# Performance work log

Hardware: AMD Instinct MI355X
Metric: run time of the kernel (lower is better)

The kernel has to match this reference:

```python
import jax, jax.numpy as jnp
import numpy as np

H = 4096        # hidden_size
NH = 32         # heads
HD = H // NH    # head_dim = 128
EPS = 1e-5
MINUS_INF = -10000.0
B, S = 2, 1024


def setup_inputs() -> dict:
    key = jax.random.key(0)
    ks = jax.random.split(key, 7)
    x = jax.random.normal(ks[0], (B, S, H), jnp.float32)
    mask = jnp.zeros((B, 1, 1, S), jnp.float32)  # additive padding mask (0 = keep)
    norm_w = 1.0 + 0.02 * jax.random.normal(ks[1], (H,), jnp.float32)
    norm_b = 0.02 * jax.random.normal(ks[2], (H,), jnp.float32)
    qkv_w = 0.02 * jax.random.normal(ks[3], (H, 3 * H), jnp.float32)
    qkv_b = 0.02 * jax.random.normal(ks[4], (3 * H,), jnp.float32)
    attn_ow = 0.02 * jax.random.normal(ks[5], (H, H), jnp.float32)
    return {"x": x, "mask": mask, "norm_w": norm_w, "norm_b": norm_b,
            "qkv_w": qkv_w, "qkv_b": qkv_b, "attn_ow": attn_ow}


def reference(x, mask, norm_w, norm_b, qkv_w, qkv_b, attn_ow):
    b, s, h = x.shape
    # --- pre-attention layernorm (qkv_gemm fuses this in DeepSpeed) ---
    mu = jnp.mean(x, axis=-1, keepdims=True)
    var = jnp.mean(jnp.square(x - mu), axis=-1, keepdims=True)
    inp_norm = (x - mu) * jax.lax.rsqrt(var + EPS) * norm_w + norm_b
    # --- fused QKV GEMM + bias ---
    qkv = inp_norm @ qkv_w + qkv_b                      # [b, s, 3H]
    q, k, v = jnp.split(qkv, 3, axis=-1)
    q = q.reshape(b, s, NH, HD).transpose(0, 2, 1, 3)   # [b, nh, s, hd]
    k = k.reshape(b, s, NH, HD).transpose(0, 2, 1, 3)
    v = v.reshape(b, s, NH, HD).transpose(0, 2, 1, 3)
    # --- scaled dot-product with triangular (causal) mask + additive input mask ---
    norm_factor = 1.0 / jnp.sqrt(jnp.asarray(HD, x.dtype))
    scores = jnp.einsum('bhqd,bhkd->bhqk', q, k) * norm_factor  # [b, nh, s, s]
    causal = jnp.where(jnp.tril(jnp.ones((s, s), bool)), 0.0, MINUS_INF).astype(x.dtype)
    probs = jax.nn.softmax(scores + causal + mask, axis=-1)
    ctx = jnp.einsum('bhqk,bhkd->bhqd', probs, v)               # [b, nh, s, hd]
    ctx = ctx.transpose(0, 2, 1, 3).reshape(b, s, h)
    # --- output projection (vector_matmul, bias applied later in MLP residual-add) ---
    out = ctx @ attn_ow
    return out
```

## Files before the change

### kernel.cpp

```cpp
#include <hip/hip_runtime.h>
#include <stdint.h>


#define S_LEN 1024
#define HID   4096
#define NHEAD 32
#define HDIM  128

typedef __attribute__((ext_vector_type(8))) short bf16x8;
typedef __attribute__((ext_vector_type(4))) float f32x4;
typedef __attribute__((ext_vector_type(8))) unsigned short us8;

__device__ __forceinline__ unsigned short f2bf(float f) {
    union { float f; unsigned u; } v; v.f = f;
    unsigned r = v.u + 0x7fffu + ((v.u >> 16) & 1u);
    return (unsigned short)(r >> 16);
}

__device__ __forceinline__ void gld16(const unsigned short* g, unsigned short* l) {
    __builtin_amdgcn_global_load_lds(
        (const __attribute__((address_space(1))) void*)g,
        (__attribute__((address_space(3))) void*)l, 16, 0, 0);
}

__global__ __launch_bounds__(256) void ln_kernel(const float* __restrict__ x,
        const float* __restrict__ w, const float* __restrict__ bch,
        unsigned short* __restrict__ out) {
    const int row = blockIdx.x;
    const int t = threadIdx.x;
    const float* xr = x + (size_t)row * HID;
    float4 v[4];
    float sum = 0.f, sq = 0.f;
#pragma unroll
    for (int i = 0; i < 4; i++) {
        v[i] = ((const float4*)xr)[t + (i << 8)];
        sum += v[i].x + v[i].y + v[i].z + v[i].w;
        sq  += v[i].x*v[i].x + v[i].y*v[i].y + v[i].z*v[i].z + v[i].w*v[i].w;
    }
#pragma unroll
    for (int off = 32; off; off >>= 1) {
        sum += __shfl_down(sum, off);
        sq  += __shfl_down(sq, off);
    }
    __shared__ float ssum[4], ssq[4];
    if ((t & 63) == 0) { ssum[t >> 6] = sum; ssq[t >> 6] = sq; }
    __syncthreads();
    const float s_all = ssum[0] + ssum[1] + ssum[2] + ssum[3];
    const float q_all = ssq[0] + ssq[1] + ssq[2] + ssq[3];
    const float mean = s_all * (1.f / HID);
    const float var  = q_all * (1.f / HID) - mean * mean;
    const float rstd = rsqrtf(var + 1e-5f);
    unsigned short* orow = out + (size_t)row * HID;
#pragma unroll
    for (int i = 0; i < 4; i++) {
        float4 wv = ((const float4*)w)[t + (i << 8)];
        float4 bv = ((const float4*)bch)[t + (i << 8)];
        ushort4 o;
        o.x = f2bf((v[i].x - mean) * rstd * wv.x + bv.x);
        o.y = f2bf((v[i].y - mean) * rstd * wv.y + bv.y);
        o.z = f2bf((v[i].z - mean) * rstd * wv.z + bv.z);
        o.w = f2bf((v[i].w - mean) * rstd * wv.w + bv.w);
        ((ushort4*)orow)[t + (i << 8)] = o;
    }
}

__global__ __launch_bounds__(256) void transconv(const float* __restrict__ W,
        unsigned short* __restrict__ Wt, int K, int N) {
    __shared__ float tileT[128 * 65];
    const int n0 = blockIdx.x << 7, k0 = blockIdx.y << 6;
    const int t = threadIdx.x;
#pragma unroll
    for (int it = 0; it < 8; it++) {
        int idx = (it << 8) + t;
        int r = idx >> 5;
        int c4 = idx & 31;
        float4 v = *(const float4*)(W + (size_t)(k0 + r) * N + n0 + (c4 << 2));
        tileT[((c4 << 2) + 0) * 65 + r] = v.x;
        tileT[((c4 << 2) + 1) * 65 + r] = v.y;
        tileT[((c4 << 2) + 2) * 65 + r] = v.z;
        tileT[((c4 << 2) + 3) * 65 + r] = v.w;
    }
    __syncthreads();
#pragma unroll
    for (int it = 0; it < 4; it++) {
        int idx = (it << 8) + t;
        int n = idx >> 3;
        int k8 = idx & 7;
        const float* src = &tileT[n * 65 + (k8 << 3)];
        us8 o;
#pragma unroll
        for (int e = 0; e < 8; e++) o[e] = f2bf(src[e]);
        *(us8*)(Wt + (size_t)(n0 + n) * K + k0 + (k8 << 3)) = o;
    }
}


#define QK_TILE(TT, CURB, PFB)                                                    \
  {                                                                               \
    int pf_ = (TT) + 2; if (pf_ > 127) pf_ = 127;                                 \
    stgA(pf_, PFB); stgB(pf_, PFB);                                               \
    bf16x8 bfv[3], af[8];                                                         \
    _Pragma("unroll") for (int jj = 0; jj < 3; jj++) bfv[jj] = ldB(CURB, jj);     \
    _Pragma("unroll") for (int ii = 0; ii < 8; ii++) af[ii] = ldA(CURB, ii);      \
    __builtin_amdgcn_s_setprio(1);                                                \
    _Pragma("unroll") for (int ii = 0; ii < 8; ii++)                              \
      _Pragma("unroll") for (int jj = 0; jj < 3; jj++)                            \
        acc[ii][jj] = __builtin_amdgcn_mfma_f32_16x16x32_bf16(                    \
            af[ii], bfv[jj], acc[ii][jj], 0, 0, 0);                               \
    __builtin_amdgcn_s_setprio(0);                                                \
    if (wave < 4) { asm volatile("s_waitcnt vmcnt(4)" ::: "memory"); }            \
    else          { asm volatile("s_waitcnt vmcnt(3)" ::: "memory"); }            \
    __builtin_amdgcn_s_barrier();                                                 \
  }

__global__ __launch_bounds__(512, 2) void gemm_qkv32(
        const unsigned short* __restrict__ A,
        const unsigned short* __restrict__ Bt,
        const float* __restrict__ bias,
        unsigned short* __restrict__ qb,
        unsigned short* __restrict__ kb,
        unsigned short* __restrict__ vt) {
    __shared__ unsigned short lds[43008];
    const int orig = blockIdx.x;
    const int bm = orig & 7, bn = orig >> 3;
    const int t = threadIdx.x;
    const int wave = t >> 6, lane = t & 63, quad = lane >> 4, l16 = lane & 15;
    const int waveM = wave >> 2, waveN = wave & 3;

    const unsigned short* GA = A  + ((size_t)bm << 8) * HID;
    const unsigned short* GB = Bt + ((size_t)bn * 192) * HID;

    const int swz  = (((lane & 3) ^ ((lane >> 3) & 3)) << 3);
    const int arow = lane >> 2;

    auto stgA = [&](int tt, int buf) {
#pragma unroll
        for (int u = 0; u < 2; u++) {
            const int g = (wave << 1) + u;
            gld16(GA + (size_t)((g << 4) + arow) * HID + (tt << 5) + swz,
                  lds + buf * 14336 + (g << 9));
        }
    };
    auto stgB = [&](int tt, int buf) {
        if (wave < 4) {
#pragma unroll
            for (int u = 0; u < 2; u++) {
                const int g = (wave << 1) + u;
                gld16(GB + (size_t)((g << 4) + arow) * HID + (tt << 5) + swz,
                      lds + buf * 14336 + 8192 + (g << 9));
            }
        } else {
            const int g = wave + 4;
            gld16(GB + (size_t)((g << 4) + arow) * HID + (tt << 5) + swz,
                  lds + buf * 14336 + 8192 + (g << 9));
        }
    };
    auto ldA = [&](int buf, int i) -> bf16x8 {
        const int r = (waveM << 7) + (i << 4) + l16;
        return ((const bf16x8*)lds)
            [((buf * 14336) >> 3) + (r << 2) + (quad ^ ((r >> 1) & 3))];
    };
    auto ldB = [&](int buf, int j) -> bf16x8 {
        const int r = waveN * 48 + (j << 4) + l16;
        return ((const bf16x8*)lds)
            [((buf * 14336 + 8192) >> 3) + (r << 2) + (quad ^ ((r >> 1) & 3))];
    };

    const f32x4 fz = {0.f, 0.f, 0.f, 0.f};
    f32x4 acc[8][3];
#pragma unroll
    for (int i = 0; i < 8; i++)
#pragma unroll
        for (int j = 0; j < 3; j++) acc[i][j] = fz;

    stgA(0, 0); stgB(0, 0);
    stgA(1, 1); stgB(1, 1);
    if (wave < 4) { asm volatile("s_waitcnt vmcnt(4)" ::: "memory"); }
    else          { asm volatile("s_waitcnt vmcnt(3)" ::: "memory"); }
    __builtin_amdgcn_s_barrier();

    for (int tt = 0; tt < 126; tt += 3) {
        QK_TILE(tt,     0, 2)
        QK_TILE(tt + 1, 1, 0)
        QK_TILE(tt + 2, 2, 1)
    }
    QK_TILE(126, 0, 2)
    QK_TILE(127, 1, 0)
    asm volatile("s_waitcnt vmcnt(0)" ::: "memory");

#pragma unroll
    for (int ii = 0; ii < 8; ii++) {
#pragma unroll
        for (int jj = 0; jj < 3; jj++) {
#pragma unroll
            for (int r = 0; r < 4; r++) {
                int m = (bm << 8) + (waveM << 7) + (ii << 4) + (quad << 2) + r;
                int n = bn * 192 + waveN * 48 + (jj << 4) + l16;
                float v = acc[ii][jj][r] + bias[n];
                unsigned short bvv = f2bf(v);
                int bb = m >> 10, s = m & 1023;
                int which = n >> 12;
                int h = n & 4095, head = h >> 7, hd = h & 127;
                size_t bh = (size_t)(bb << 5) + head;
                if (which == 0)      qb[(bh * S_LEN + s) * HDIM + hd] = bvv;
                else if (which == 1) kb[(bh * S_LEN + s) * HDIM + hd] = bvv;
                else                 vt[(bh * HDIM + hd) * S_LEN + s] = bvv;
            }
        }
    }
}


#define PJ_TILE(TT, CURB, PFB)                                                    \
  {                                                                               \
    int pf_ = (TT) + 2; if (pf_ > 127) pf_ = 127;                                 \
    stgA(pf_, PFB); stgB(pf_, PFB);                                               \
    bf16x8 bfv[4], af[4];                                                         \
    _Pragma("unroll") for (int jj = 0; jj < 4; jj++) bfv[jj] = ldB(CURB, jj);     \
    _Pragma("unroll") for (int ii = 0; ii < 4; ii++) af[ii] = ldA(CURB, ii);      \
    __builtin_amdgcn_s_setprio(1);                                                \
    _Pragma("unroll") for (int ii = 0; ii < 4; ii++)                              \
      _Pragma("unroll") for (int jj = 0; jj < 4; jj++)                            \
        acc[ii][jj] = __builtin_amdgcn_mfma_f32_16x16x32_bf16(                    \
            af[ii], bfv[jj], acc[ii][jj], 0, 0, 0);                               \
    __builtin_amdgcn_s_setprio(0);                                                \
    asm volatile("s_waitcnt vmcnt(3)" ::: "memory");                              \
    __builtin_amdgcn_s_barrier();                                                 \
  }

__global__ __launch_bounds__(512, 2) void gemm_proj32(
        const unsigned short* __restrict__ A,
        const unsigned short* __restrict__ Bt,
        float* __restrict__ outf) {
    __shared__ unsigned short lds[36864];
    const int orig = blockIdx.x;
    const int bm = orig & 7, bn = orig >> 3;
    const int t = threadIdx.x;
    const int wave = t >> 6, lane = t & 63, quad = lane >> 4, l16 = lane & 15;
    const int waveM = wave >> 1, waveN = wave & 1;

    const unsigned short* GA = A  + ((size_t)bm << 8) * HID;
    const unsigned short* GB = Bt + ((size_t)bn << 7) * HID;

    const int swz  = (((lane & 3) ^ ((lane >> 3) & 3)) << 3);
    const int arow = lane >> 2;

    auto stgA = [&](int tt, int buf) {
#pragma unroll
        for (int u = 0; u < 2; u++) {
            const int g = (wave << 1) + u;
            gld16(GA + (size_t)((g << 4) + arow) * HID + (tt << 5) + swz,
                  lds + buf * 12288 + (g << 9));
        }
    };
    auto stgB = [&](int tt, int buf) {
        const int g = wave;
        gld16(GB + (size_t)((g << 4) + arow) * HID + (tt << 5) + swz,
              lds + buf * 12288 + 8192 + (g << 9));
    };
    auto ldA = [&](int buf, int i) -> bf16x8 {
        const int r = (waveM << 6) + (i << 4) + l16;
        return ((const bf16x8*)lds)
            [((buf * 12288) >> 3) + (r << 2) + (quad ^ ((r >> 1) & 3))];
    };
    auto ldB = [&](int buf, int j) -> bf16x8 {
        const int r = (waveN << 6) + (j << 4) + l16;
        return ((const bf16x8*)lds)
            [((buf * 12288 + 8192) >> 3) + (r << 2) + (quad ^ ((r >> 1) & 3))];
    };

    const f32x4 fz = {0.f, 0.f, 0.f, 0.f};
    f32x4 acc[4][4];
#pragma unroll
    for (int i = 0; i < 4; i++)
#pragma unroll
        for (int j = 0; j < 4; j++) acc[i][j] = fz;

    stgA(0, 0); stgB(0, 0);
    stgA(1, 1); stgB(1, 1);
    asm volatile("s_waitcnt vmcnt(3)" ::: "memory");
    __builtin_amdgcn_s_barrier();

    for (int tt = 0; tt < 126; tt += 3) {
        PJ_TILE(tt,     0, 2)
        PJ_TILE(tt + 1, 1, 0)
        PJ_TILE(tt + 2, 2, 1)
    }
    PJ_TILE(126, 0, 2)
    PJ_TILE(127, 1, 0)
    asm volatile("s_waitcnt vmcnt(0)" ::: "memory");

#pragma unroll
    for (int ii = 0; ii < 4; ii++)
#pragma unroll
        for (int jj = 0; jj < 4; jj++)
#pragma unroll
            for (int r = 0; r < 4; r++) {
                int m = (bm << 8) + (waveM << 6) + (ii << 4) + (quad << 2) + r;
                int n = (bn << 7) + (waveN << 6) + (jj << 4) + l16;
                outf[((size_t)m << 12) + n] = acc[ii][jj][r];
            }
}

__global__ __launch_bounds__(256) void attn_kernel(
        const unsigned short* __restrict__ qbuf,
        const unsigned short* __restrict__ kbuf,
        const unsigned short* __restrict__ vtbuf,
        const float* __restrict__ mask,
        unsigned short* __restrict__ ctx) {
    __shared__ unsigned short q_lds[64 * 128];
    __shared__ unsigned short k_lds[64 * 128];
    __shared__ unsigned short v_lds[128 * 64];
    __shared__ unsigned short p_lds[64 * 64];
    const int t = threadIdx.x;
    const int wave = t >> 6, lane = t & 63, quad = lane >> 4, l16 = lane & 15;
    const int bq = blockIdx.x, bh = blockIdx.y;
    const int q0 = bq << 6;
    const int b = bh >> 5;
    const unsigned short* Q  = qbuf  + (size_t)bh * S_LEN * HDIM;
    const unsigned short* Kp = kbuf  + (size_t)bh * S_LEN * HDIM;
    const unsigned short* Vp = vtbuf + (size_t)bh * HDIM * S_LEN;

    {
        int r = t >> 4;
        int c = (((t & 15) ^ ((t >> 4) & 7)) << 3);
#pragma unroll
        for (int it = 0; it < 4; it++)
            gld16(Q + (size_t)(q0 + r + (it << 4)) * HDIM + c,
                  q_lds + ((((it << 8) + (wave << 6))) << 3));
    }

    const f32x4 fz = {0.f, 0.f, 0.f, 0.f};
    f32x4 o[8];
#pragma unroll
    for (int n = 0; n < 8; n++) o[n] = fz;
    float l_i[4] = {0.f, 0.f, 0.f, 0.f};
    const float scale = 0.08838834764831845f;
    const float* mrow = mask + b * S_LEN;

    for (int kt = 0; kt <= bq; kt++) {
        const int k0 = kt << 6;
        {
            int rk = t >> 4, ck = (((t & 15) ^ ((t >> 4) & 7)) << 3);
            int rv = t >> 3, cv = (((t & 7) ^ ((t >> 3) & 7)) << 3);
#pragma unroll
            for (int it = 0; it < 4; it++) {
                gld16(Kp + (size_t)(k0 + rk + (it << 4)) * HDIM + ck,
                      k_lds + (((it << 8) + (wave << 6)) << 3));
                gld16(Vp + (size_t)(rv + (it << 5)) * S_LEN + k0 + cv,
                      v_lds + (((it << 8) + (wave << 6)) << 3));
            }
        }
        __syncthreads();

        f32x4 sacc[4];
#pragma unroll
        for (int j = 0; j < 4; j++) sacc[j] = fz;
        const bf16x8* qv = (const bf16x8*)q_lds;
        const bf16x8* kv = (const bf16x8*)k_lds;
#pragma unroll
        for (int kk = 0; kk < 4; kk++) {
            bf16x8 aq = qv[(((wave << 4) + l16) << 4) + (((kk << 2) + quad) ^ (l16 & 7))];
#pragma unroll
            for (int j = 0; j < 4; j++) {
                bf16x8 bk = kv[((((j << 4) + l16)) << 4) + (((kk << 2) + quad) ^ (l16 & 7))];
                sacc[j] = __builtin_amdgcn_mfma_f32_16x16x32_bf16(aq, bk, sacc[j], 0, 0, 0);
            }
        }

#pragma unroll
        for (int r = 0; r < 4; r++) {
            int prow = (wave << 4) + (quad << 2) + r;
            int qrow = q0 + prow;
#pragma unroll
            for (int j = 0; j < 4; j++) {
                int key = k0 + (j << 4) + l16;
                float x = sacc[j][r] * scale + mrow[key];
                if (key > qrow) x -= 10000.0f;
                float p = __expf(x);
                l_i[r] += p;
                int pc = (j << 1) + (l16 >> 3);
                p_lds[(prow << 6) + ((pc ^ (prow & 7)) << 3) + (l16 & 7)] = f2bf(p);
            }
        }
        __syncthreads();

        const bf16x8* pvv = (const bf16x8*)p_lds;
        const bf16x8* vv = (const bf16x8*)v_lds;
#pragma unroll
        for (int ks = 0; ks < 2; ks++) {
            bf16x8 ap = pvv[(((wave << 4) + l16) << 3) + (((ks << 2) + quad) ^ (l16 & 7))];
#pragma unroll
            for (int n = 0; n < 8; n++) {
                bf16x8 bvv = vv[((((n << 4) + l16)) << 3) + (((ks << 2) + quad) ^ (l16 & 7))];
                o[n] = __builtin_amdgcn_mfma_f32_16x16x32_bf16(ap, bvv, o[n], 0, 0, 0);
            }
        }
        __syncthreads();
    }

#pragma unroll
    for (int r = 0; r < 4; r++) {
        float l = l_i[r];
#pragma unroll
        for (int off = 1; off < 16; off <<= 1) l += __shfl_xor(l, off);
        float inv = 1.0f / l;
        int qrow = q0 + (wave << 4) + (quad << 2) + r;
        size_t base = ((size_t)(b * S_LEN + qrow)) * HID + ((size_t)(bh & 31) << 7);
#pragma unroll
        for (int n = 0; n < 8; n++)
            ctx[base + (n << 4) + l16] = f2bf(o[n][r] * inv);
    }
}

extern "C" void kernel_launch(void* const* d_in, const int* in_sizes, int n_in,
                              void* d_out, int out_size, void* d_ws, size_t ws_size,
                              hipStream_t stream) {
    const float* x       = (const float*)d_in[0];
    const float* mask    = (const float*)d_in[1];
    const float* norm_w  = (const float*)d_in[2];
    const float* norm_b  = (const float*)d_in[3];
    const float* qkv_w   = (const float*)d_in[4];
    const float* qkv_b   = (const float*)d_in[5];
    const float* attn_ow = (const float*)d_in[6];
    float* out = (float*)d_out;

    char* ws = (char*)d_ws;
    size_t off = 0;
    auto alloc = [&](size_t bytes) {
        char* p = ws + off;
        off += (bytes + 255) & ~(size_t)255;
        return p;
    };
    unsigned short* inp_norm = (unsigned short*)alloc((size_t)2048 * HID * 2);
    unsigned short* qkv_wt   = (unsigned short*)alloc((size_t)3 * HID * HID * 2);
    unsigned short* ow_t     = (unsigned short*)alloc((size_t)HID * HID * 2);
    unsigned short* qb       = (unsigned short*)alloc((size_t)64 * S_LEN * HDIM * 2);
    unsigned short* kb       = (unsigned short*)alloc((size_t)64 * S_LEN * HDIM * 2);
    unsigned short* vt       = (unsigned short*)alloc((size_t)64 * S_LEN * HDIM * 2);
    unsigned short* ctx      = (unsigned short*)alloc((size_t)2048 * HID * 2);

    ln_kernel<<<2048, 256, 0, stream>>>(x, norm_w, norm_b, inp_norm);
    transconv<<<dim3(3 * HID / 128, HID / 64), 256, 0, stream>>>(qkv_w, qkv_wt, HID, 3 * HID);
    transconv<<<dim3(HID / 128, HID / 64), 256, 0, stream>>>(attn_ow, ow_t, HID, HID);
    gemm_qkv32<<<512, 512, 0, stream>>>(inp_norm, qkv_wt, qkv_b, qb, kb, vt);
    attn_kernel<<<dim3(16, 64), 256, 0, stream>>>(qb, kb, vt, mask, ctx);
    gemm_proj32<<<256, 512, 0, stream>>>(ctx, ow_t, out);
}
```

Baseline: 715.4 us.

## Widen QKV GEMM block tile to 256x384 with split B-fragment loads

The QKV GEMM block tile grows from 256x192 to 256x384, which halves the grid to 256 blocks and doubles the per-wave accumulator count to 8x6. The inner step now loads A fragments once and reuses them across two half-passes over B fragments, so each A tile is fetched from global memory and LDS fewer times. LDS per block and accumulator register pressure both rise. With 256 blocks on a 256-CU device this may leave one block per CU and reduce latency hiding, and spilling is possible under the 2-wave launch bound.

```diff
diff --git a/kernel.cpp b/kernel.cpp
--- a/kernel.cpp
+++ b/kernel.cpp
@@ -95,32 +95,38 @@
 }
 
 
-#define QK_TILE(TT, CURB, PFB)                                                    \
+#define QK_STEP(TT, CURB, PFB)                                                    \
   {                                                                               \
     int pf_ = (TT) + 2; if (pf_ > 127) pf_ = 127;                                 \
     stgA(pf_, PFB); stgB(pf_, PFB);                                               \
-    bf16x8 bfv[3], af[8];                                                         \
+    bf16x8 af[8], bfv[3];                                                         \
+    _Pragma("unroll") for (int ii = 0; ii < 8; ii++) af[ii] = ldA(CURB, ii);      \
     _Pragma("unroll") for (int jj = 0; jj < 3; jj++) bfv[jj] = ldB(CURB, jj);     \
-    _Pragma("unroll") for (int ii = 0; ii < 8; ii++) af[ii] = ldA(CURB, ii);      \
     __builtin_amdgcn_s_setprio(1);                                                \
-    _Pragma("unroll") for (int ii = 0; ii < 8; ii++)                              \
-      _Pragma("unroll") for (int jj = 0; jj < 3; jj++)                            \
+    _Pragma("unroll") for (int jj = 0; jj < 3; jj++)                              \
+      _Pragma("unroll") for (int ii = 0; ii < 8; ii++)                            \
         acc[ii][jj] = __builtin_amdgcn_mfma_f32_16x16x32_bf16(                    \
             af[ii], bfv[jj], acc[ii][jj], 0, 0, 0);                               \
     __builtin_amdgcn_s_setprio(0);                                                \
-    if (wave < 4) { asm volatile("s_waitcnt vmcnt(4)" ::: "memory"); }            \
-    else          { asm volatile("s_waitcnt vmcnt(3)" ::: "memory"); }            \
+    _Pragma("unroll") for (int jj = 0; jj < 3; jj++) bfv[jj] = ldB(CURB, jj + 3); \
+    __builtin_amdgcn_s_setprio(1);                                                \
+    _Pragma("unroll") for (int jj = 0; jj < 3; jj++)                              \
+      _Pragma("unroll") for (int ii = 0; ii < 8; ii++)                            \
+        acc[ii][jj + 3] = __builtin_amdgcn_mfma_f32_16x16x32_bf16(                \
+            af[ii], bfv[jj], acc[ii][jj + 3], 0, 0, 0);                           \
+    __builtin_amdgcn_s_setprio(0);                                                \
+    asm volatile("s_waitcnt vmcnt(5)" ::: "memory");                              \
     __builtin_amdgcn_s_barrier();                                                 \
   }
 
-__global__ __launch_bounds__(512, 2) void gemm_qkv32(
+__global__ __launch_bounds__(512, 2) void gemm_qkv384(
         const unsigned short* __restrict__ A,
         const unsigned short* __restrict__ Bt,
         const float* __restrict__ bias,
         unsigned short* __restrict__ qb,
         unsigned short* __restrict__ kb,
         unsigned short* __restrict__ vt) {
-    __shared__ unsigned short lds[43008];
+    __shared__ unsigned short lds[61440];
     const int orig = blockIdx.x;
     const int bm = orig & 7, bn = orig >> 3;
     const int t = threadIdx.x;
@@ -128,7 +134,7 @@
     const int waveM = wave >> 2, waveN = wave & 3;
 
     const unsigned short* GA = A  + ((size_t)bm << 8) * HID;
-    const unsigned short* GB = Bt + ((size_t)bn * 192) * HID;
+    const unsigned short* GB = Bt + ((size_t)bn * 384) * HID;
 
     const int swz  = (((lane & 3) ^ ((lane >> 3) & 3)) << 3);
     const int arow = lane >> 2;
@@ -138,64 +144,57 @@
         for (int u = 0; u < 2; u++) {
             const int g = (wave << 1) + u;
             gld16(GA + (size_t)((g << 4) + arow) * HID + (tt << 5) + swz,
-                  lds + buf * 14336 + (g << 9));
+                  lds + buf * 20480 + (g << 9));
         }
     };
     auto stgB = [&](int tt, int buf) {
-        if (wave < 4) {
-#pragma unroll
-            for (int u = 0; u < 2; u++) {
-                const int g = (wave << 1) + u;
-                gld16(GB + (size_t)((g << 4) + arow) * HID + (tt << 5) + swz,
-                      lds + buf * 14336 + 8192 + (g << 9));
-            }
-        } else {
-            const int g = wave + 4;
+#pragma unroll
+        for (int u = 0; u < 3; u++) {
+            const int g = wave * 3 + u;
             gld16(GB + (size_t)((g << 4) + arow) * HID + (tt << 5) + swz,
-                  lds + buf * 14336 + 8192 + (g << 9));
+                  lds + buf * 20480 + 8192 + (g << 9));
         }
     };
     auto ldA = [&](int buf, int i) -> bf16x8 {
         const int r = (waveM << 7) + (i << 4) + l16;
         return ((const bf16x8*)lds)
-            [((buf * 14336) >> 3) + (r << 2) + (quad ^ ((r >> 1) & 3))];
+            [buf * 2560 + (r << 2) + (quad ^ ((r >> 1) & 3))];
     };
     auto ldB = [&](int buf, int j) -> bf16x8 {
-        const int r = waveN * 48 + (j << 4) + l16;
+        const int r = waveN * 96 + (j << 4) + l16;
         return ((const bf16x8*)lds)
-            [((buf * 14336 + 8192) >> 3) + (r << 2) + (quad ^ ((r >> 1) & 3))];
+            [buf * 2560 + 1024 + (r << 2) + (quad ^ ((r >> 1) & 3))];
     };
 
     const f32x4 fz = {0.f, 0.f, 0.f, 0.f};
-    f32x4 acc[8][3];
+    f32x4 acc[8][6];
 #pragma unroll
     for (int i = 0; i < 8; i++)
 #pragma unroll
-        for (int j = 0; j < 3; j++) acc[i][j] = fz;
+        for (int j = 0; j < 6; j++) acc[i][j] = fz;
 
     stgA(0, 0); stgB(0, 0);
     stgA(1, 1); stgB(1, 1);
-    if (wave < 4) { asm volatile("s_waitcnt vmcnt(4)" ::: "memory"); }
-    else          { asm volatile("s_waitcnt vmcnt(3)" ::: "memory"); }
+    asm volatile("s_waitcnt vmcnt(5)" ::: "memory");
     __builtin_amdgcn_s_barrier();
 
     for (int tt = 0; tt < 126; tt += 3) {
-        QK_TILE(tt,     0, 2)
-        QK_TILE(tt + 1, 1, 0)
-        QK_TILE(tt + 2, 2, 1)
-    }
-    QK_TILE(126, 0, 2)
-    QK_TILE(127, 1, 0)
+        QK_STEP(tt,     0, 2)
+        QK_STEP(tt + 1, 1, 0)
+        QK_STEP(tt + 2, 2, 1)
+    }
+    QK_STEP(126, 0, 2)
+    QK_STEP(127, 1, 0)
     asm volatile("s_waitcnt vmcnt(0)" ::: "memory");
 
 #pragma unroll
     for (int ii = 0; ii < 8; ii++) {
 #pragma unroll
-        for (int jj = 0; jj < 3; jj++) {
+        for (int jj = 0; jj < 6; jj++) {
 #pragma unroll
             for (int r = 0; r < 4; r++) {
                 int m = (bm << 8) + (waveM << 7) + (ii << 4) + (quad << 2) + r;
-                int n = bn * 192 + waveN * 48 + (jj << 4) + l16;
+                int n = bn * 384 + waveN * 96 + (jj << 4) + l16;
                 float v = acc[ii][jj][r] + bias[n];
                 unsigned short bvv = f2bf(v);
                 int bb = m >> 10, s = m & 1023;
@@ -443,7 +442,7 @@
     ln_kernel<<<2048, 256, 0, stream>>>(x, norm_w, norm_b, inp_norm);
     transconv<<<dim3(3 * HID / 128, HID / 64), 256, 0, stream>>>(qkv_w, qkv_wt, HID, 3 * HID);
     transconv<<<dim3(HID / 128, HID / 64), 256, 0, stream>>>(attn_ow, ow_t, HID, HID);
-    gemm_qkv32<<<512, 512, 0, stream>>>(inp_norm, qkv_wt, qkv_b, qb, kb, vt);
+    gemm_qkv384<<<256, 512, 0, stream>>>(inp_norm, qkv_wt, qkv_b, qb, kb, vt);
     attn_kernel<<<dim3(16, 64), 256, 0, stream>>>(qb, kb, vt, mask, ctx);
     gemm_proj32<<<256, 512, 0, stream>>>(ctx, ow_t, out);
 }
```

After: 1.035 ms. 44.6% more time.
